# Kernel optimization log

Hardware: AMD Instinct MI355X
Metric: run time of the kernel (lower is better)

The kernel has to match this reference:

```python
import jax, jax.numpy as jnp
import numpy as np

DIM = 256
NUM_HEADS = 4
HEAD_DIM = DIM // NUM_HEADS
LN_EPS = 1e-5


def setup_inputs() -> dict:
    key = jax.random.key(0)
    ks = jax.random.split(key, 5)
    B, C, H, W = 4, DIM, 64, 64
    x = jax.random.normal(ks[0], (B, C, H, W), dtype=jnp.float32)
    ln_g = jnp.ones((DIM,), dtype=jnp.float32)
    ln_b = jnp.zeros((DIM,), dtype=jnp.float32)
    # torch Linear init scale ~ 1/sqrt(fan_in)
    w_qkv = jax.random.normal(ks[1], (DIM, 3 * DIM), dtype=jnp.float32) / np.sqrt(DIM)
    w_proj = jax.random.normal(ks[2], (DIM, DIM), dtype=jnp.float32) / np.sqrt(DIM)
    b_proj = jax.random.normal(ks[3], (DIM,), dtype=jnp.float32) * 0.01
    return {"x": x, "ln_g": ln_g, "ln_b": ln_b, "w_qkv": w_qkv,
            "w_proj": w_proj, "b_proj": b_proj}


def _attention_block(x, ln_g, ln_b, w_qkv, w_proj, b_proj):
    B, C, H, W = x.shape
    N = H * W
    h, d = NUM_HEADS, HEAD_DIM
    # b c h w -> b n c
    t = x.reshape(B, C, N).transpose(0, 2, 1)
    # LayerNorm over channel dim
    mu = jnp.mean(t, axis=-1, keepdims=True)
    var = jnp.mean(jnp.square(t - mu), axis=-1, keepdims=True)
    t = (t - mu) * jax.lax.rsqrt(var + LN_EPS) * ln_g + ln_b
    # qkv projection (no bias); layout of last dim is (three, heads, d)
    qkv = t @ w_qkv  # [B, N, 3*C]
    qkv = qkv.reshape(B, N, 3, h, d)
    q = qkv[:, :, 0].transpose(0, 2, 1, 3)  # [B, h, N, d]
    k = qkv[:, :, 1].transpose(0, 2, 1, 3)
    v = qkv[:, :, 2].transpose(0, 2, 1, 3)
    # scaled dot-product attention (original chunks over queries; same math)
    scale = 1.0 / jnp.sqrt(jnp.asarray(d, dtype=q.dtype))
    dots = jnp.einsum('bhnd,bhmd->bhnm', q, k) * scale
    attn = jax.nn.softmax(dots, axis=-1)
    o = jnp.einsum('bhnm,bhmd->bhnd', attn, v)  # [B, h, N, d]
    # b h n d -> b n (h d)
    o = o.transpose(0, 2, 1, 3).reshape(B, N, C)
    o = o @ w_proj.T + b_proj  # torch Linear convention not needed; keep explicit
    # b n c -> b c h w
    return o.transpose(0, 2, 1).reshape(B, C, H, W)


def reference(x, ln_g, ln_b, w_qkv, w_proj, b_proj):
    return _attention_block(x, ln_g, ln_b, w_qkv, w_proj, b_proj)
```

## Files before the change

### kernel.cpp

```cpp
#include <hip/hip_runtime.h>
#include <math.h>

#define NB 4
#define NC 256
#define NHEADS 4
#define DH 64
#define NT 4096
#define QSCALE (0.125f * 1.44269504088896f)

typedef __bf16  bf16x8 __attribute__((ext_vector_type(8)));
typedef float   f32x4  __attribute__((ext_vector_type(4)));
typedef float   f32x16 __attribute__((ext_vector_type(16)));
typedef short   s16x8  __attribute__((ext_vector_type(8)));
typedef unsigned int u32x4 __attribute__((ext_vector_type(4)));

static __device__ __forceinline__ unsigned short f2bf(float f) {
    unsigned u = __float_as_uint(f);
    u = (u + 0x7fffu + ((u >> 16) & 1u)) >> 16;
    return (unsigned short)u;
}

static __device__ __forceinline__ float fast_exp2(float x) {
    return __builtin_amdgcn_exp2f(x);
}

static __device__ __forceinline__ unsigned cvtpk(float lo, float hi) {
    unsigned r;
    asm("v_cvt_pk_bf16_f32 %0, %1, %2" : "=v"(r) : "v"(lo), "v"(hi));
    return r;
}

static __device__ __forceinline__ void plswap(unsigned &a, unsigned &b) {
    asm("v_permlane32_swap_b32 %0, %1" : "+v"(a), "+v"(b));
}

static __device__ __forceinline__ bf16x8 as_bf16x8(u32x4 v) {
    return __builtin_bit_cast(bf16x8, v);
}

static __device__ __forceinline__ void gload16(const unsigned short* g, unsigned short* l) {
    __builtin_amdgcn_global_load_lds((const __attribute__((address_space(1))) void*)g,
                                     (__attribute__((address_space(3))) void*)l, 16, 0, 0);
}

static __device__ __forceinline__ void stage_64x256(
    unsigned short* __restrict__ lds, const unsigned short* __restrict__ g, int tid)
{
    #pragma unroll
    for (int chunk = 0; chunk < 8; ++chunk) {
        const int row = chunk * 8 + (tid >> 5);
        const int col = (tid & 31) * 8;
        *(s16x8*)&lds[row * 264 + col] = *(const s16x8*)&g[row * 256 + col];
    }
}

__global__ __launch_bounds__(256) void k_prep(
    const float* __restrict__ wqkv, const float* __restrict__ wproj,
    unsigned short* __restrict__ wqkv_t, unsigned short* __restrict__ wproj_bf)
{
    const int id = blockIdx.x;
    const int tid = threadIdx.x;
    if (id < 48) {
        __shared__ float T[64][65];
        const int jt = id % 12, ct = id / 12;
        #pragma unroll
        for (int p = 0; p < 16; ++p) {
            const int idx = tid + (p << 8);
            const int r = idx >> 6, cl = idx & 63;
            T[r][cl] = wqkv[(size_t)(ct * 64 + r) * 768 + jt * 64 + cl];
        }
        __syncthreads();
        #pragma unroll
        for (int p = 0; p < 16; ++p) {
            const int idx = tid + (p << 8);
            const int r = idx >> 6, cl = idx & 63;
            wqkv_t[(size_t)(jt * 64 + r) * 256 + ct * 64 + cl] = f2bf(T[cl][r]);
        }
    } else {
        const int base = (id - 48) * 2048 + tid * 8;
        s16x8 v;
        #pragma unroll
        for (int j = 0; j < 8; ++j) v[j] = (short)f2bf(wproj[base + j]);
        *(s16x8*)&wproj_bf[base] = v;
    }
}

__global__ __launch_bounds__(256) void k_ln_qkv(
    const float* __restrict__ x,
    const float* __restrict__ ln_g,
    const float* __restrict__ ln_b,
    const unsigned short* __restrict__ wqkv_t,
    unsigned short* __restrict__ q_bf,
    unsigned short* __restrict__ k_bf,
    unsigned short* __restrict__ v_bf)
{
    __shared__ unsigned short An[64 * 264];
    __shared__ unsigned short Wt[64 * 264];
    __shared__ float red1[4][64], red2[4][64];
    __shared__ float mu_s[64], rs_s[64];

    const int b     = blockIdx.x >> 6;
    const int n0    = (blockIdx.x & 63) << 6;
    const int three = blockIdx.y;
    const int tid   = threadIdx.x;
    const int li    = tid & 63;
    const int grp   = tid >> 6;
    const int w     = grp;
    const int lane  = li;
    const int q4    = lane >> 4;
    const int c     = lane & 15;

    const float* xb = x + ((size_t)b * NC) * NT + n0 + li;

    float xr[64];
    #pragma unroll
    for (int chunk = 0; chunk < 8; ++chunk)
        #pragma unroll
        for (int j = 0; j < 8; ++j)
            xr[chunk * 8 + j] = xb[(size_t)(chunk * 32 + grp * 8 + j) * NT];

    float s1 = 0.f, s2 = 0.f;
    #pragma unroll
    for (int i = 0; i < 64; ++i) { s1 += xr[i]; s2 += xr[i] * xr[i]; }
    red1[grp][li] = s1; red2[grp][li] = s2;
    __syncthreads();
    if (tid < 64) {
        const float t1 = red1[0][tid] + red1[1][tid] + red1[2][tid] + red1[3][tid];
        const float t2 = red2[0][tid] + red2[1][tid] + red2[2][tid] + red2[3][tid];
        const float mu  = t1 * (1.0f / NC);
        const float var = t2 * (1.0f / NC) - mu * mu;
        mu_s[tid] = mu;
        rs_s[tid] = rsqrtf(var + 1e-5f);
    }
    __syncthreads();
    const float mu = mu_s[li];
    const float rs = rs_s[li];

    #pragma unroll
    for (int chunk = 0; chunk < 8; ++chunk) {
        s16x8 pk;
        #pragma unroll
        for (int j = 0; j < 8; ++j) {
            const int ch = chunk * 32 + grp * 8 + j;
            const float vv = (xr[chunk * 8 + j] - mu) * rs * ln_g[ch] + ln_b[ch];
            pk[j] = (short)f2bf(vv);
        }
        *(s16x8*)&An[li * 264 + chunk * 32 + grp * 8] = pk;
    }
    __syncthreads();

    bf16x8 aT[8];
    if (three < 2) {
        #pragma unroll
        for (int kt = 0; kt < 8; ++kt)
            aT[kt] = *(const bf16x8*)&An[(16 * w + c) * 264 + kt * 32 + q4 * 8];
    }

    for (int jt = 0; jt < 4; ++jt) {
        __syncthreads();
        stage_64x256(Wt, wqkv_t + (size_t)(three * 256 + jt * 64) * 256, tid);
        __syncthreads();

        f32x4 acc[4];
        #pragma unroll
        for (int nt = 0; nt < 4; ++nt)
            #pragma unroll
            for (int r = 0; r < 4; ++r) acc[nt][r] = 0.f;

        const int bh = b * NHEADS + jt;
        if (three < 2) {
            #pragma unroll
            for (int nt = 0; nt < 4; ++nt)
                #pragma unroll
                for (int kt = 0; kt < 8; ++kt) {
                    const bf16x8 bb = *(const bf16x8*)&Wt[(16 * nt + c) * 264 + kt * 32 + q4 * 8];
                    acc[nt] = __builtin_amdgcn_mfma_f32_16x16x32_bf16(aT[kt], bb, acc[nt], 0, 0, 0);
                }
            unsigned short* dst = (three == 0 ? q_bf : k_bf) + ((size_t)bh * NT + n0) * DH;
            const float sc = (three == 0) ? QSCALE : 1.0f;
            #pragma unroll
            for (int nt = 0; nt < 4; ++nt)
                #pragma unroll
                for (int r = 0; r < 4; ++r)
                    dst[(size_t)(16 * w + 4 * q4 + r) * DH + 16 * nt + c] = f2bf(acc[nt][r] * sc);
        } else {
            bf16x8 aW[8];
            #pragma unroll
            for (int kt = 0; kt < 8; ++kt)
                aW[kt] = *(const bf16x8*)&Wt[(16 * w + c) * 264 + kt * 32 + q4 * 8];
            #pragma unroll
            for (int nt = 0; nt < 4; ++nt)
                #pragma unroll
                for (int kt = 0; kt < 8; ++kt) {
                    const bf16x8 bb = *(const bf16x8*)&An[(16 * nt + c) * 264 + kt * 32 + q4 * 8];
                    acc[nt] = __builtin_amdgcn_mfma_f32_16x16x32_bf16(aW[kt], bb, acc[nt], 0, 0, 0);
                }
            unsigned short* dst = v_bf + (size_t)bh * DH * NT;
            #pragma unroll
            for (int nt = 0; nt < 4; ++nt)
                #pragma unroll
                for (int r = 0; r < 4; ++r)
                    dst[(size_t)(16 * w + 4 * q4 + r) * NT + n0 + 16 * nt + c] = f2bf(acc[nt][r]);
        }
    }
}

__global__ __launch_bounds__(256, 2) void k_attn(
    const unsigned short* __restrict__ qg,
    const unsigned short* __restrict__ kg,
    const unsigned short* __restrict__ vg,
    unsigned short* __restrict__ og)
{
    __shared__ unsigned short Ks[2 * 8192];
    __shared__ unsigned short Vt[2 * 8192];
    __shared__ float l_s[4][32];

    const int bx   = ((blockIdx.x & 7) << 6) | (blockIdx.x >> 3);
    const int bh   = bx >> 5;
    const int qt   = bx & 31;
    const int n0   = qt << 7;
    const int tid  = threadIdx.x;
    const int w    = tid >> 6;
    const int lane = tid & 63;
    const int c5   = lane & 31;
    const int hi   = lane >> 5;
    const int qb   = n0 + (w << 5);
    const int swz  = c5 & 7;

    const unsigned short* kb = kg + (size_t)bh * NT * DH;
    const unsigned short* vb = vg + (size_t)bh * DH * NT;

    bf16x8 aq[4];
    {
        const unsigned short* qrow = qg + ((size_t)bh * NT + qb + c5) * DH + hi * 8;
        #pragma unroll
        for (int ks = 0; ks < 4; ++ks)
            aq[ks] = *(const bf16x8*)(qrow + ks * 16);
    }

    const int rr  = lane >> 3;
    const int kcK = (lane & 7) ^ rr;
    const int rd  = lane >> 4;
    const int ckV = lane & 15;

    #define ISSUE_TILE(it_, bi_)                                               \
        {                                                                      \
            const unsigned short* ktp = kb + (size_t)(it_) * 128 * DH;         \
            const unsigned short* vtp = vb + (size_t)(it_) * 128;              \
            _Pragma("unroll")                                                  \
            for (int t = 0; t < 4; ++t) {                                      \
                const int grp_ = w * 4 + t;                                    \
                gload16(ktp + (size_t)(grp_ * 8 + rr) * DH + kcK * 8,          \
                        &Ks[(bi_) * 8192 + grp_ * 512 + lane * 8]);            \
                const int kcV_ = ckV ^ ((4 * grp_ + rd) & 7);                  \
                gload16(vtp + (size_t)(4 * grp_ + rd) * NT + kcV_ * 8,         \
                        &Vt[(bi_) * 8192 + grp_ * 512 + lane * 8]);            \
            }                                                                  \
        }

    ISSUE_TILE(0, 0)

    f32x16 oac[2];
    #pragma unroll
    for (int dt = 0; dt < 2; ++dt)
        #pragma unroll
        for (int r = 0; r < 16; ++r) oac[dt][r] = 0.f;
    float ls0 = 0.f, ls1 = 0.f, ls2 = 0.f, ls3 = 0.f;

    for (int it = 0; it < 32; ++it) {
        const int cur = it & 1;
        asm volatile("s_waitcnt vmcnt(0)\n\ts_barrier" ::: "memory");
        if (it < 31) ISSUE_TILE(it + 1, cur ^ 1)

        const unsigned short* Kb = &Ks[cur * 8192];
        const unsigned short* Vb = &Vt[cur * 8192];

        #pragma unroll
        for (int hf = 0; hf < 2; ++hf) {
            const int sb0 = 2 * hf, sb1 = 2 * hf + 1;

            f32x16 s0, s1;
            #pragma unroll
            for (int r = 0; r < 16; ++r) { s0[r] = 0.f; s1[r] = 0.f; }
            __builtin_amdgcn_s_setprio(1);
            #pragma unroll
            for (int ks = 0; ks < 4; ++ks) {
                const bf16x8 kf0 = *(const bf16x8*)
                    &Kb[(sb0 * 32 + c5) * 64 + (((2 * ks + hi) ^ swz) << 3)];
                s0 = __builtin_amdgcn_mfma_f32_32x32x16_bf16(kf0, aq[ks], s0, 0, 0, 0);
            }
            #pragma unroll
            for (int ks = 0; ks < 4; ++ks) {
                const bf16x8 kf1 = *(const bf16x8*)
                    &Kb[(sb1 * 32 + c5) * 64 + (((2 * ks + hi) ^ swz) << 3)];
                s1 = __builtin_amdgcn_mfma_f32_32x32x16_bf16(kf1, aq[ks], s1, 0, 0, 0);
            }
            __builtin_amdgcn_s_setprio(0);

            #pragma unroll
            for (int r = 0; r < 16; r += 4) {
                s0[r]   = fast_exp2(s0[r]);   ls0 += s0[r];
                s0[r+1] = fast_exp2(s0[r+1]); ls1 += s0[r+1];
                s0[r+2] = fast_exp2(s0[r+2]); ls2 += s0[r+2];
                s0[r+3] = fast_exp2(s0[r+3]); ls3 += s0[r+3];
            }
            #pragma unroll
            for (int r = 0; r < 16; r += 4) {
                s1[r]   = fast_exp2(s1[r]);   ls0 += s1[r];
                s1[r+1] = fast_exp2(s1[r+1]); ls1 += s1[r+1];
                s1[r+2] = fast_exp2(s1[r+2]); ls2 += s1[r+2];
                s1[r+3] = fast_exp2(s1[r+3]); ls3 += s1[r+3];
            }

            unsigned A0 = cvtpk(s0[0],  s0[1]),  A1 = cvtpk(s0[4],  s0[5]);
            plswap(A0, A1);
            unsigned A2 = cvtpk(s0[2],  s0[3]),  A3 = cvtpk(s0[6],  s0[7]);
            plswap(A2, A3);
            const u32x4 paA0 = (u32x4){A0, A2, A1, A3};
            unsigned B0 = cvtpk(s0[8],  s0[9]),  B1 = cvtpk(s0[12], s0[13]);
            plswap(B0, B1);
            unsigned B2 = cvtpk(s0[10], s0[11]), B3 = cvtpk(s0[14], s0[15]);
            plswap(B2, B3);
            const u32x4 paB0 = (u32x4){B0, B2, B1, B3};
            unsigned C0 = cvtpk(s1[0],  s1[1]),  C1 = cvtpk(s1[4],  s1[5]);
            plswap(C0, C1);
            unsigned C2 = cvtpk(s1[2],  s1[3]),  C3 = cvtpk(s1[6],  s1[7]);
            plswap(C2, C3);
            const u32x4 paA1 = (u32x4){C0, C2, C1, C3};
            unsigned D0 = cvtpk(s1[8],  s1[9]),  D1 = cvtpk(s1[12], s1[13]);
            plswap(D0, D1);
            unsigned D2 = cvtpk(s1[10], s1[11]), D3 = cvtpk(s1[14], s1[15]);
            plswap(D2, D3);
            const u32x4 paB1 = (u32x4){D0, D2, D1, D3};

            __builtin_amdgcn_s_setprio(1);
            #pragma unroll
            for (int dt = 0; dt < 2; ++dt) {
                const int rv = (dt * 32 + c5) * 128;
                const bf16x8 vA0 = *(const bf16x8*)&Vb[rv + (((4*sb0 + hi) ^ swz) << 3)];
                oac[dt] = __builtin_amdgcn_mfma_f32_32x32x16_bf16(
                    as_bf16x8(paA0), vA0, oac[dt], 0, 0, 0);
                const bf16x8 vB0 = *(const bf16x8*)&Vb[rv + (((4*sb0 + 2 + hi) ^ swz) << 3)];
                oac[dt] = __builtin_amdgcn_mfma_f32_32x32x16_bf16(
                    as_bf16x8(paB0), vB0, oac[dt], 0, 0, 0);
                const bf16x8 vA1 = *(const bf16x8*)&Vb[rv + (((4*sb1 + hi) ^ swz) << 3)];
                oac[dt] = __builtin_amdgcn_mfma_f32_32x32x16_bf16(
                    as_bf16x8(paA1), vA1, oac[dt], 0, 0, 0);
                const bf16x8 vB1 = *(const bf16x8*)&Vb[rv + (((4*sb1 + 2 + hi) ^ swz) << 3)];
                oac[dt] = __builtin_amdgcn_mfma_f32_32x32x16_bf16(
                    as_bf16x8(paB1), vB1, oac[dt], 0, 0, 0);
            }
            __builtin_amdgcn_s_setprio(0);
        }
    }
    #undef ISSUE_TILE

    const float lsum = (ls0 + ls1) + (ls2 + ls3);
    const float t = lsum + __shfl_xor(lsum, 32);
    if (lane < 32) l_s[w][c5] = t;
    __syncthreads();

    unsigned short* ob = og + ((size_t)bh * NT + qb) * DH;
    #pragma unroll
    for (int r = 0; r < 16; ++r) {
        const int qrow = (r & 3) + 8 * (r >> 2) + 4 * hi;
        const float rn = 1.0f / l_s[w][qrow];
        ob[(size_t)qrow * DH + c5]      = f2bf(oac[0][r] * rn);
        ob[(size_t)qrow * DH + 32 + c5] = f2bf(oac[1][r] * rn);
    }
}

__global__ __launch_bounds__(256) void k_proj(
    const unsigned short* __restrict__ o_bf,
    const unsigned short* __restrict__ wproj_bf,
    const float* __restrict__ b_proj,
    float* __restrict__ out)
{
    __shared__ unsigned short Os[64 * 264];
    __shared__ unsigned short Ws[64 * 264];

    const int b   = blockIdx.x >> 6;
    const int n0  = (blockIdx.x & 63) << 6;
    const int yh  = blockIdx.y;
    const int tid = threadIdx.x;
    const int w   = tid >> 6;
    const int lane = tid & 63;
    const int q4  = lane >> 4;
    const int c   = lane & 15;

    #pragma unroll
    for (int chunk = 0; chunk < 8; ++chunk) {
        const int row = chunk * 8 + (tid >> 5);
        const int col = (tid & 31) * 8;
        const int hd  = col >> 6;
        const int c64 = col & 63;
        const unsigned short* src =
            &o_bf[((size_t)(b * NHEADS + hd) * NT + n0 + row) * DH + c64];
        *(s16x8*)&Os[row * 264 + col] = *(const s16x8*)src;
    }

    for (int ct = 0; ct < 2; ++ct) {
        const int cg0 = (yh * 2 + ct) * 64;
        if (ct) __syncthreads();
        stage_64x256(Ws, wproj_bf + (size_t)cg0 * NC, tid);
        __syncthreads();

        bf16x8 a[8];
        #pragma unroll
        for (int kt = 0; kt < 8; ++kt)
            a[kt] = *(const bf16x8*)&Ws[(16 * w + c) * 264 + kt * 32 + q4 * 8];

        f32x4 acc[4];
        #pragma unroll
        for (int nt = 0; nt < 4; ++nt)
            #pragma unroll
            for (int r = 0; r < 4; ++r) acc[nt][r] = 0.f;

        #pragma unroll
        for (int nt = 0; nt < 4; ++nt)
            #pragma unroll
            for (int kt = 0; kt < 8; ++kt) {
                const bf16x8 bb = *(const bf16x8*)&Os[(16 * nt + c) * 264 + kt * 32 + q4 * 8];
                acc[nt] = __builtin_amdgcn_mfma_f32_16x16x32_bf16(a[kt], bb, acc[nt], 0, 0, 0);
            }

        #pragma unroll
        for (int nt = 0; nt < 4; ++nt)
            #pragma unroll
            for (int r = 0; r < 4; ++r) {
                const int cg = cg0 + 16 * w + 4 * q4 + r;
                out[((size_t)b * NC + cg) * NT + n0 + 16 * nt + c] = acc[nt][r] + b_proj[cg];
            }
    }
}

extern "C" void kernel_launch(void* const* d_in, const int* in_sizes, int n_in,
                              void* d_out, int out_size, void* d_ws, size_t ws_size,
                              hipStream_t stream)
{
    const float* x      = (const float*)d_in[0];
    const float* ln_g   = (const float*)d_in[1];
    const float* ln_b   = (const float*)d_in[2];
    const float* w_qkv  = (const float*)d_in[3];
    const float* w_proj = (const float*)d_in[4];
    const float* b_proj = (const float*)d_in[5];
    float* out = (float*)d_out;

    const size_t TEN = (size_t)NB * NHEADS * NT * DH;

    unsigned short* ws16 = (unsigned short*)d_ws;
    unsigned short* q_bf    = ws16;
    unsigned short* k_bf    = ws16 + TEN;
    unsigned short* v_bf    = ws16 + 2 * TEN;
    unsigned short* o_bf    = ws16 + 3 * TEN;
    unsigned short* wqkv_t  = ws16 + 4 * TEN;
    unsigned short* wproj_b = wqkv_t + 768 * 256;

    k_prep<<<80, 256, 0, stream>>>(w_qkv, w_proj, wqkv_t, wproj_b);
    k_ln_qkv<<<dim3(NB * 64, 3), 256, 0, stream>>>(x, ln_g, ln_b, wqkv_t, q_bf, k_bf, v_bf);
    k_attn<<<512, 256, 0, stream>>>(q_bf, k_bf, v_bf, o_bf);
    k_proj<<<dim3(NB * 64, 2), 256, 0, stream>>>(o_bf, wproj_b, b_proj, out);
}
```

Baseline: 181.8 us.

## Fuse Q/K/V projections into one block with double-buffered async weight loads

The LN+QKV kernel now runs one block per 64-token tile that computes all of Q, K and V. Before, three blocks each re-read x and recomputed the LayerNorm. Weight tiles are staged into a double-buffered LDS area with async global-to-LDS loads (gload16) using an XOR swizzle, so the next tile's load overlaps the current MFMA work. This removes the 3x redundant x reads and LN work, but cuts the grid from 768 to 256 blocks and raises LDS use, which may reduce parallelism.

Result: no change. 185.3 us (+2.0%).

```diff
diff --git a/kernel.cpp b/kernel.cpp
--- a/kernel.cpp
+++ b/kernel.cpp
@@ -95,13 +95,12 @@
     unsigned short* __restrict__ v_bf)
 {
     __shared__ unsigned short An[64 * 264];
-    __shared__ unsigned short Wt[64 * 264];
+    __shared__ unsigned short Wt[2][64 * 256];
     __shared__ float red1[4][64], red2[4][64];
     __shared__ float mu_s[64], rs_s[64];
 
     const int b     = blockIdx.x >> 6;
     const int n0    = (blockIdx.x & 63) << 6;
-    const int three = blockIdx.y;
     const int tid   = threadIdx.x;
     const int li    = tid & 63;
     const int grp   = tid >> 6;
@@ -109,6 +108,23 @@
     const int lane  = li;
     const int q4    = lane >> 4;
     const int c     = lane & 15;
+
+    const int wrow2  = lane >> 5;
+    const int wchunk = lane & 31;
+
+    #define ISSUE_W(idx_, buf_)                                                \
+        {                                                                      \
+            const unsigned short* wsrc = wqkv_t + (size_t)(idx_) * 64 * 256;   \
+            _Pragma("unroll")                                                  \
+            for (int t = 0; t < 8; ++t) {                                      \
+                const int g_ = w * 8 + t;                                      \
+                const int r_ = 2 * g_ + wrow2;                                 \
+                gload16(wsrc + r_ * 256 + ((wchunk ^ (r_ & 7)) << 3),          \
+                        &Wt[buf_][g_ * 512 + lane * 8]);                       \
+            }                                                                  \
+        }
+
+    ISSUE_W(0, 0)
 
     const float* xb = x + ((size_t)b * NC) * NT + n0 + li;
 
@@ -150,16 +166,17 @@
     __syncthreads();
 
     bf16x8 aT[8];
-    if (three < 2) {
-        #pragma unroll
-        for (int kt = 0; kt < 8; ++kt)
-            aT[kt] = *(const bf16x8*)&An[(16 * w + c) * 264 + kt * 32 + q4 * 8];
-    }
-
-    for (int jt = 0; jt < 4; ++jt) {
-        __syncthreads();
-        stage_64x256(Wt, wqkv_t + (size_t)(three * 256 + jt * 64) * 256, tid);
-        __syncthreads();
+    #pragma unroll
+    for (int kt = 0; kt < 8; ++kt)
+        aT[kt] = *(const bf16x8*)&An[(16 * w + c) * 264 + kt * 32 + q4 * 8];
+
+    for (int idx = 0; idx < 12; ++idx) {
+        const int buf = idx & 1;
+        asm volatile("s_waitcnt vmcnt(0)\n\ts_barrier" ::: "memory");
+        if (idx < 11) ISSUE_W(idx + 1, buf ^ 1)
+
+        const int three = idx >> 2;
+        const int jt    = idx & 3;
 
         f32x4 acc[4];
         #pragma unroll
@@ -170,12 +187,15 @@
         const int bh = b * NHEADS + jt;
         if (three < 2) {
             #pragma unroll
-            for (int nt = 0; nt < 4; ++nt)
+            for (int nt = 0; nt < 4; ++nt) {
+                const int row = 16 * nt + c;
                 #pragma unroll
                 for (int kt = 0; kt < 8; ++kt) {
-                    const bf16x8 bb = *(const bf16x8*)&Wt[(16 * nt + c) * 264 + kt * 32 + q4 * 8];
+                    const bf16x8 bb = *(const bf16x8*)
+                        &Wt[buf][row * 256 + (((4 * kt + q4) ^ (row & 7)) << 3)];
                     acc[nt] = __builtin_amdgcn_mfma_f32_16x16x32_bf16(aT[kt], bb, acc[nt], 0, 0, 0);
                 }
+            }
             unsigned short* dst = (three == 0 ? q_bf : k_bf) + ((size_t)bh * NT + n0) * DH;
             const float sc = (three == 0) ? QSCALE : 1.0f;
             #pragma unroll
@@ -185,9 +205,11 @@
                     dst[(size_t)(16 * w + 4 * q4 + r) * DH + 16 * nt + c] = f2bf(acc[nt][r] * sc);
         } else {
             bf16x8 aW[8];
+            const int wrow = 16 * w + c;
             #pragma unroll
             for (int kt = 0; kt < 8; ++kt)
-                aW[kt] = *(const bf16x8*)&Wt[(16 * w + c) * 264 + kt * 32 + q4 * 8];
+                aW[kt] = *(const bf16x8*)
+                    &Wt[buf][wrow * 256 + (((4 * kt + q4) ^ (wrow & 7)) << 3)];
             #pragma unroll
             for (int nt = 0; nt < 4; ++nt)
                 #pragma unroll
@@ -203,6 +225,7 @@
                     dst[(size_t)(16 * w + 4 * q4 + r) * NT + n0 + 16 * nt + c] = f2bf(acc[nt][r]);
         }
     }
+    #undef ISSUE_W
 }
 
 __global__ __launch_bounds__(256, 2) void k_attn(
@@ -457,7 +480,7 @@
     unsigned short* wproj_b = wqkv_t + 768 * 256;
 
     k_prep<<<80, 256, 0, stream>>>(w_qkv, w_proj, wqkv_t, wproj_b);
-    k_ln_qkv<<<dim3(NB * 64, 3), 256, 0, stream>>>(x, ln_g, ln_b, wqkv_t, q_bf, k_bf, v_bf);
+    k_ln_qkv<<<NB * 64, 256, 0, stream>>>(x, ln_g, ln_b, wqkv_t, q_bf, k_bf, v_bf);
     k_attn<<<512, 256, 0, stream>>>(q_bf, k_bf, v_bf, o_bf);
     k_proj<<<dim3(NB * 64, 2), 256, 0, stream>>>(o_bf, wproj_b, b_proj, out);
 }
```

## Fuse q/k/v projections into one block and register-prefetch weight tiles

Applied to the files above, without the earlier changes.

The LN+QKV kernel now has each block compute all three projections (q, k, v) across 12 weight tiles instead of launching three blocks per token tile. This removes the redundant x loading and LayerNorm work that was repeated three times. Weight tiles are prefetched into registers one tile ahead, so the next global load overlaps with the MFMA work on the current LDS tile. The projection kernel gets the same register double-buffering for its two weight tiles. In exchange, the grid has a third as many blocks, which cuts parallelism, and the extra wreg registers raise register pressure.

Measured after the change: 185.7 us. 1.02x slower.

```diff
diff --git a/kernel.cpp b/kernel.cpp
--- a/kernel.cpp
+++ b/kernel.cpp
@@ -41,17 +41,6 @@
 static __device__ __forceinline__ void gload16(const unsigned short* g, unsigned short* l) {
     __builtin_amdgcn_global_load_lds((const __attribute__((address_space(1))) void*)g,
                                      (__attribute__((address_space(3))) void*)l, 16, 0, 0);
-}
-
-static __device__ __forceinline__ void stage_64x256(
-    unsigned short* __restrict__ lds, const unsigned short* __restrict__ g, int tid)
-{
-    #pragma unroll
-    for (int chunk = 0; chunk < 8; ++chunk) {
-        const int row = chunk * 8 + (tid >> 5);
-        const int col = (tid & 31) * 8;
-        *(s16x8*)&lds[row * 264 + col] = *(const s16x8*)&g[row * 256 + col];
-    }
 }
 
 __global__ __launch_bounds__(256) void k_prep(
@@ -101,7 +90,6 @@
 
     const int b     = blockIdx.x >> 6;
     const int n0    = (blockIdx.x & 63) << 6;
-    const int three = blockIdx.y;
     const int tid   = threadIdx.x;
     const int li    = tid & 63;
     const int grp   = tid >> 6;
@@ -109,6 +97,25 @@
     const int lane  = li;
     const int q4    = lane >> 4;
     const int c     = lane & 15;
+
+    const int srow = tid >> 5;
+    const int scol = (tid & 31) * 8;
+    s16x8 wreg[8];
+    #define WLOAD(idx_)                                                        \
+        {                                                                      \
+            const unsigned short* wsrc = wqkv_t + (size_t)(idx_) * 64 * 256;   \
+            _Pragma("unroll")                                                  \
+            for (int ch = 0; ch < 8; ++ch)                                     \
+                wreg[ch] = *(const s16x8*)&wsrc[(ch * 8 + srow) * 256 + scol]; \
+        }
+    #define WSTORE                                                             \
+        {                                                                      \
+            _Pragma("unroll")                                                  \
+            for (int ch = 0; ch < 8; ++ch)                                     \
+                *(s16x8*)&Wt[(ch * 8 + srow) * 264 + scol] = wreg[ch];         \
+        }
+
+    WLOAD(0)
 
     const float* xb = x + ((size_t)b * NC) * NT + n0 + li;
 
@@ -150,16 +157,18 @@
     __syncthreads();
 
     bf16x8 aT[8];
-    if (three < 2) {
-        #pragma unroll
-        for (int kt = 0; kt < 8; ++kt)
-            aT[kt] = *(const bf16x8*)&An[(16 * w + c) * 264 + kt * 32 + q4 * 8];
-    }
-
-    for (int jt = 0; jt < 4; ++jt) {
+    #pragma unroll
+    for (int kt = 0; kt < 8; ++kt)
+        aT[kt] = *(const bf16x8*)&An[(16 * w + c) * 264 + kt * 32 + q4 * 8];
+
+    for (int idx = 0; idx < 12; ++idx) {
+        if (idx) __syncthreads();
+        WSTORE
+        if (idx < 11) WLOAD(idx + 1)
         __syncthreads();
-        stage_64x256(Wt, wqkv_t + (size_t)(three * 256 + jt * 64) * 256, tid);
-        __syncthreads();
+
+        const int three = idx >> 2;
+        const int jt    = idx & 3;
 
         f32x4 acc[4];
         #pragma unroll
@@ -203,6 +212,8 @@
                     dst[(size_t)(16 * w + 4 * q4 + r) * NT + n0 + 16 * nt + c] = f2bf(acc[nt][r]);
         }
     }
+    #undef WLOAD
+    #undef WSTORE
 }
 
 __global__ __launch_bounds__(256, 2) void k_attn(
@@ -388,6 +399,25 @@
     const int q4  = lane >> 4;
     const int c   = lane & 15;
 
+    const int srow = tid >> 5;
+    const int scol = (tid & 31) * 8;
+    s16x8 wreg[8];
+    #define WLOADP(cg0_)                                                       \
+        {                                                                      \
+            const unsigned short* wsrc = wproj_bf + (size_t)(cg0_) * NC;       \
+            _Pragma("unroll")                                                  \
+            for (int ch = 0; ch < 8; ++ch)                                     \
+                wreg[ch] = *(const s16x8*)&wsrc[(ch * 8 + srow) * 256 + scol]; \
+        }
+    #define WSTOREP                                                            \
+        {                                                                      \
+            _Pragma("unroll")                                                  \
+            for (int ch = 0; ch < 8; ++ch)                                     \
+                *(s16x8*)&Ws[(ch * 8 + srow) * 264 + scol] = wreg[ch];         \
+        }
+
+    WLOADP(yh * 128)
+
     #pragma unroll
     for (int chunk = 0; chunk < 8; ++chunk) {
         const int row = chunk * 8 + (tid >> 5);
@@ -402,7 +432,8 @@
     for (int ct = 0; ct < 2; ++ct) {
         const int cg0 = (yh * 2 + ct) * 64;
         if (ct) __syncthreads();
-        stage_64x256(Ws, wproj_bf + (size_t)cg0 * NC, tid);
+        WSTOREP
+        if (ct == 0) WLOADP(yh * 128 + 64)
         __syncthreads();
 
         bf16x8 a[8];
@@ -432,6 +463,8 @@
                 out[((size_t)b * NC + cg) * NT + n0 + 16 * nt + c] = acc[nt][r] + b_proj[cg];
             }
     }
+    #undef WLOADP
+    #undef WSTOREP
 }
 
 extern "C" void kernel_launch(void* const* d_in, const int* in_sizes, int n_in,
@@ -457,7 +490,7 @@
     unsigned short* wproj_b = wqkv_t + 768 * 256;
 
     k_prep<<<80, 256, 0, stream>>>(w_qkv, w_proj, wqkv_t, wproj_b);
-    k_ln_qkv<<<dim3(NB * 64, 3), 256, 0, stream>>>(x, ln_g, ln_b, wqkv_t, q_bf, k_bf, v_bf);
+    k_ln_qkv<<<NB * 64, 256, 0, stream>>>(x, ln_g, ln_b, wqkv_t, q_bf, k_bf, v_bf);
     k_attn<<<512, 256, 0, stream>>>(q_bf, k_bf, v_bf, o_bf);
     k_proj<<<dim3(NB * 64, 2), 256, 0, stream>>>(o_bf, wproj_b, b_proj, out);
 }
```
